# Kernel tuning notes

Hardware: AMD Instinct MI355X
Metric: run time of the kernel (lower is better)

Reference implementation:

```python
import jax, jax.numpy as jnp
import numpy as np

B, S, D = 4, 2048, 1024
H = 16
DH = D // H
MLP_DIM = 4096
EPS = 1e-6


def setup_inputs() -> dict:
    key = jax.random.key(0)
    ks = jax.random.split(key, 16)
    sd = lambda fi, fo: (1.0 / np.sqrt(fi))
    return {
        "x": jax.random.normal(ks[0], (B, S, D), jnp.float32),
        "Wq": jax.random.normal(ks[1], (D, D), jnp.float32) * sd(D, D),
        "bq": jnp.zeros((D,), jnp.float32),
        "Wk": jax.random.normal(ks[2], (D, D), jnp.float32) * sd(D, D),
        "bk": jnp.zeros((D,), jnp.float32),
        "Wv": jax.random.normal(ks[3], (D, D), jnp.float32) * sd(D, D),
        "bv": jnp.zeros((D,), jnp.float32),
        "Wo": jax.random.normal(ks[4], (D, D), jnp.float32) * sd(D, D),
        "bo": jnp.zeros((D,), jnp.float32),
        "ln1_g": jnp.ones((D,), jnp.float32),
        "ln1_b": jnp.zeros((D,), jnp.float32),
        "ln2_g": jnp.ones((D,), jnp.float32),
        "ln2_b": jnp.zeros((D,), jnp.float32),
        "W1": jax.random.normal(ks[5], (D, MLP_DIM), jnp.float32) * sd(D, MLP_DIM),
        "b1": jax.random.normal(ks[6], (MLP_DIM,), jnp.float32) * 1e-6,
        "W2": jax.random.normal(ks[7], (MLP_DIM, D), jnp.float32) * sd(MLP_DIM, D),
        "b2": jax.random.normal(ks[8], (D,), jnp.float32) * 1e-6,
    }


def _layernorm(x, g, b):
    mu = jnp.mean(x, axis=-1, keepdims=True)
    var = jnp.mean(jnp.square(x - mu), axis=-1, keepdims=True)
    return (x - mu) * jax.lax.rsqrt(var + EPS) * g + b


def reference(x, Wq, bq, Wk, bk, Wv, bv, Wo, bo,
              ln1_g, ln1_b, ln2_g, ln2_b, W1, b1, W2, b2):
    h = x
    xn = _layernorm(x, ln1_g, ln1_b)
    # Q/K/V: [B,S,D] -> [B,H,S,DH]
    def split_heads(t):
        return t.reshape(B, S, H, DH).transpose(0, 2, 1, 3)
    Q = split_heads(xn @ Wq + bq)
    K = split_heads(xn @ Wk + bk)
    V = split_heads(xn @ Wv + bv)
    scores = jnp.einsum("bhqd,bhkd->bhqk", Q, K) / np.sqrt(DH).astype(np.float32)
    a = jax.nn.softmax(scores, axis=-1)
    r = jnp.einsum("bhqk,bhkd->bhqd", a, V)          # [B,H,S,DH]
    r = r.transpose(0, 2, 1, 3).reshape(B, S, D)      # merge heads
    r = r @ Wo + bo
    x = r + h
    h = x
    xn = _layernorm(x, ln2_g, ln2_b)
    m = jax.nn.gelu(xn @ W1 + b1, approximate=False)
    m = m @ W2 + b2
    return m + h
```

## Files before the change

kernel.cpp:

```cpp
#include <hip/hip_runtime.h>
#include <math.h>

#define B_ 4
#define S_ 2048
#define D_ 1024
#define H_ 16
#define MLP_ 4096
#define MROWS 8192

typedef __attribute__((ext_vector_type(4))) float f32x4;
typedef __attribute__((ext_vector_type(8))) __bf16 bf16x8;
typedef __attribute__((ext_vector_type(4))) __bf16 bf16x4;
typedef __attribute__((ext_vector_type(8))) unsigned short us8;
typedef unsigned short u16;
typedef unsigned int u32;

__device__ __forceinline__ void gload16(const void* g, void* l) {
    __builtin_amdgcn_global_load_lds((const __attribute__((address_space(1))) u32*)g,
                                     (__attribute__((address_space(3))) u32*)l, 16, 0, 0);
}

__device__ __forceinline__ float gelu_f(float v) {
    return 0.5f * v * (1.0f + erff(v * 0.70710678118654752f));
}

__global__ __launch_bounds__(256) void ln_bf16_k(const float* __restrict__ x,
                                                 const float* __restrict__ g,
                                                 const float* __restrict__ b,
                                                 u16* __restrict__ y) {
    int row = blockIdx.x;
    int tid = threadIdx.x;
    const float* xr = x + (size_t)row * D_;
    f32x4 v = *(const f32x4*)(xr + tid * 4);
    float s = v.x + v.y + v.z + v.w;
    float ss = v.x * v.x + v.y * v.y + v.z * v.z + v.w * v.w;
    for (int off = 32; off > 0; off >>= 1) {
        s += __shfl_down(s, off, 64);
        ss += __shfl_down(ss, off, 64);
    }
    __shared__ float rs[4], rss[4];
    int lane = tid & 63, wid = tid >> 6;
    if (lane == 0) { rs[wid] = s; rss[wid] = ss; }
    __syncthreads();
    s = rs[0] + rs[1] + rs[2] + rs[3];
    ss = rss[0] + rss[1] + rss[2] + rss[3];
    float mu = s * (1.0f / D_);
    float var = ss * (1.0f / D_) - mu * mu;
    float inv = rsqrtf(var + 1e-6f);
    f32x4 gg = *(const f32x4*)(g + tid * 4);
    f32x4 bb = *(const f32x4*)(b + tid * 4);
    bf16x4 o = {(__bf16)((v.x - mu) * inv * gg.x + bb.x),
                (__bf16)((v.y - mu) * inv * gg.y + bb.y),
                (__bf16)((v.z - mu) * inv * gg.z + bb.z),
                (__bf16)((v.w - mu) * inv * gg.w + bb.w)};
    *(bf16x4*)(y + (size_t)row * D_ + tid * 4) = o;
}

__global__ void pack3_k(const float* __restrict__ a, const float* __restrict__ b,
                        const float* __restrict__ c, float* __restrict__ o) {
    const float* s = blockIdx.x == 0 ? a : (blockIdx.x == 1 ? b : c);
    o[blockIdx.x * 1024 + threadIdx.x] = s[threadIdx.x];
}

__global__ __launch_bounds__(256) void wtrans_k(const float* __restrict__ W,
                                                u16* __restrict__ Wt, int K, int N) {
    __shared__ float T[32][33];
    int tid = threadIdx.x;
    int k0 = blockIdx.y * 32, n0 = blockIdx.x * 32;
    int r = tid >> 3, c4 = (tid & 7) * 4;
    f32x4 v = *(const f32x4*)&W[(size_t)(k0 + r) * N + n0 + c4];
    T[r][c4 + 0] = v.x; T[r][c4 + 1] = v.y; T[r][c4 + 2] = v.z; T[r][c4 + 3] = v.w;
    __syncthreads();
    int n = tid >> 3, kk = (tid & 7) * 4;
    bf16x4 o = {(__bf16)T[kk + 0][n], (__bf16)T[kk + 1][n],
                (__bf16)T[kk + 2][n], (__bf16)T[kk + 3][n]};
    *(bf16x4*)&Wt[(size_t)(n0 + n) * K + k0 + kk] = o;
}

__global__ __launch_bounds__(256) void vtrans_k(const u16* __restrict__ QKV,
                                                u16* __restrict__ Vt) {
    __shared__ u16 T[64][80];
    int tid = threadIdx.x;
    int s0 = blockIdx.x * 64;
    int bh = blockIdx.y, b = bh >> 4, h = bh & 15;
    int r = tid >> 2, c0 = (tid & 3) * 16;
    const u16* src = QKV + (size_t)(b * S_ + s0 + r) * 3072 + 2048 + h * 64 + c0;
    us8 v0 = *(const us8*)src;
    us8 v1 = *(const us8*)(src + 8);
    *(us8*)&T[r][c0] = v0;
    *(us8*)&T[r][c0 + 8] = v1;
    __syncthreads();
    int dh = tid >> 2, s8 = (tid & 3) * 16;
    us8 o0, o1;
#pragma unroll
    for (int i = 0; i < 8; ++i) { o0[i] = T[s8 + i][dh]; o1[i] = T[s8 + 8 + i][dh]; }
    u16* dst = Vt + (size_t)(bh * 64 + dh) * S_ + s0 + s8;
    *(us8*)dst = o0;
    *(us8*)(dst + 8) = o1;
}

template <int EPI>
__global__ __launch_bounds__(256) void gemm_bf16(const u16* __restrict__ A,
                                                 const u16* __restrict__ Wt,
                                                 const float* __restrict__ bias,
                                                 const float* __restrict__ res,
                                                 void* __restrict__ Cout,
                                                 int M, int N, int K) {
    __shared__ u16 As[3][128 * 32];
    __shared__ u16 Bs[3][128 * 32];
    const int tid = threadIdx.x;
    const int lane = tid & 63;
    const int w = tid >> 6;
    const int nwg = gridDim.x * gridDim.y;
    int hw = blockIdx.x + gridDim.x * blockIdx.y;
    int lg = (hw & 7) * (nwg >> 3) + (hw >> 3);
    const int row0 = (lg / gridDim.x) * 128;
    const int col0 = (lg % gridDim.x) * 128;
    const int l15 = lane & 15, l16 = lane >> 4;
    const int wr = w >> 1, wc = w & 1;

    f32x4 acc[4][4];
#pragma unroll
    for (int i = 0; i < 4; ++i)
#pragma unroll
        for (int j = 0; j < 4; ++j) acc[i][j] = (f32x4){0.f, 0.f, 0.f, 0.f};

    const int srow = w * 32 + (lane >> 2);
    const size_t sboff = (size_t)(lane & 3) * 16;
    const char* Ag = (const char*)A + ((size_t)(row0 + srow) * K) * 2 + sboff;
    const char* Bg = (const char*)Wt + ((size_t)(col0 + srow) * K) * 2 + sboff;
    const size_t rstep = (size_t)16 * K * 2;
    const int woff = w * 2048;
    const int T = K >> 5;

#define STAGE(t, bi) do {                                      \
        size_t kb = (size_t)(t) << 6;                          \
        char* asw = (char*)As + (bi) * 8192 + woff;            \
        char* bsw = (char*)Bs + (bi) * 8192 + woff;            \
        gload16(Ag + kb, asw);                                 \
        gload16(Ag + kb + rstep, asw + 1024);                  \
        gload16(Bg + kb, bsw);                                 \
        gload16(Bg + kb + rstep, bsw + 1024);                  \
    } while (0)

    STAGE(0, 0);
    STAGE(1, 1);
    asm volatile("s_waitcnt vmcnt(4)" ::: "memory");
    __builtin_amdgcn_s_barrier();
    __builtin_amdgcn_sched_barrier(0);

    int bi = 0;
    for (int t = 0; t < T; ++t) {
        if (t + 2 < T) {
            int nb = bi + 2; if (nb >= 3) nb -= 3;
            STAGE(t + 2, nb);
        }
        const char* Ab = (const char*)As + bi * 8192;
        const char* Bb = (const char*)Bs + bi * 8192;
        bf16x8 af[4], bfr[4];
#pragma unroll
        for (int f = 0; f < 4; ++f) {
            af[f] = *(const bf16x8*)(Ab + (size_t)(wr * 64 + f * 16 + l15) * 64 + (l16 << 4));
            bfr[f] = *(const bf16x8*)(Bb + (size_t)(wc * 64 + f * 16 + l15) * 64 + (l16 << 4));
        }
        __builtin_amdgcn_s_setprio(1);
#pragma unroll
        for (int fi = 0; fi < 4; ++fi)
#pragma unroll
            for (int fj = 0; fj < 4; ++fj)
                acc[fi][fj] = __builtin_amdgcn_mfma_f32_16x16x32_bf16(af[fi], bfr[fj], acc[fi][fj], 0, 0, 0);
        __builtin_amdgcn_s_setprio(0);
        if (t + 2 < T) {
            asm volatile("s_waitcnt vmcnt(4)" ::: "memory");
        } else {
            asm volatile("s_waitcnt vmcnt(0)" ::: "memory");
        }
        __builtin_amdgcn_s_barrier();
        __builtin_amdgcn_sched_barrier(0);
        if (++bi >= 3) bi = 0;
    }
#undef STAGE

    const int rb = row0 + wr * 64 + (l16 << 2);
    const int cb = col0 + wc * 64 + l15;
#pragma unroll
    for (int fi = 0; fi < 4; ++fi)
#pragma unroll
        for (int fj = 0; fj < 4; ++fj) {
            int c = cb + fj * 16;
            float bv = bias[c];
#pragma unroll
            for (int rr = 0; rr < 4; ++rr) {
                int r = rb + fi * 16 + rr;
                float v = acc[fi][fj][rr] + bv;
                if (EPI == 1) v = gelu_f(v);
                if (EPI == 2) {
                    v += res[(size_t)r * N + c];
                    ((float*)Cout)[(size_t)r * N + c] = v;
                } else {
                    ((__bf16*)Cout)[(size_t)r * N + c] = (__bf16)v;
                }
            }
        }
}

__global__ __launch_bounds__(256) void attn_mfma(const u16* __restrict__ QKV,
                                                 const u16* __restrict__ Vt,
                                                 u16* __restrict__ O) {
    __shared__ u16 Ks[2][64 * 64];
    __shared__ u16 Vs[2][64 * 64];
    __shared__ u16 Ps[4][16 * 64];
    const int tid = threadIdx.x, lane = tid & 63, w = tid >> 6;
    int hw = blockIdx.x + gridDim.x * blockIdx.y;
    int lg = (hw & 7) * 256 + (hw >> 3);
    const int bh = lg >> 5, b = bh >> 4, h = bh & 15;
    const int q0 = (lg & 31) * 64;
    const int l15 = lane & 15, l16 = lane >> 4;

    const u16* Qp = QKV + (size_t)(b * S_ + q0 + w * 16 + l15) * 3072 + h * 64 + (l16 << 3);
    bf16x8 qf0 = *(const bf16x8*)Qp;
    bf16x8 qf1 = *(const bf16x8*)(Qp + 32);

    f32x4 oacc[4];
#pragma unroll
    for (int i = 0; i < 4; ++i) oacc[i] = (f32x4){0.f, 0.f, 0.f, 0.f};
    float mold_l = -1e30f, lsum_l = 0.f;

    const int sr = lane >> 3;
    const size_t soff = (size_t)(((lane & 7) ^ sr) << 4);
    const char* Kg = (const char*)QKV + ((size_t)b * S_ * 3072 + 1024 + h * 64) * 2;
    const char* Vg = (const char*)Vt + (size_t)bh * 64 * S_ * 2;
    char* Pw = (char*)Ps[w];
    const float C2 = 0.18033688011112f;
    const float THRRAW = 44.0f;

    const char* kp0 = Kg + (size_t)(w * 16 + sr) * 6144 + soff;
    const char* kp1 = kp0 + 8 * 6144;
    const char* vp0 = Vg + (size_t)(w * 16 + sr) * 4096 + soff;
    const char* vp1 = vp0 + 8 * 4096;
    const size_t KADV = 64 * 6144;
    const size_t VADV = 128;
    char* ksA = (char*)Ks[0] + w * 2048;
    char* ksB = (char*)Ks[1] + w * 2048;
    char* vsA = (char*)Vs[0] + w * 2048;
    char* vsB = (char*)Vs[1] + w * 2048;

    gload16(kp0, ksA); gload16(kp1, ksA + 1024);
    gload16(vp0, vsA); gload16(vp1, vsA + 1024);
    kp0 += KADV; kp1 += KADV; vp0 += VADV; vp1 += VADV;
    __syncthreads();

    for (int kt = 0; kt < S_ / 64; ++kt) {
        const int cur = kt & 1;
        if (kt < S_ / 64 - 1) {
            char* kd = cur ? ksA : ksB;
            char* vd = cur ? vsA : vsB;
            gload16(kp0, kd); gload16(kp1, kd + 1024);
            gload16(vp0, vd); gload16(vp1, vd + 1024);
            kp0 += KADV; kp1 += KADV; vp0 += VADV; vp1 += VADV;
        }

        f32x4 sfr[4];
        const char* Kb_ = (const char*)Ks[cur];
        __builtin_amdgcn_s_setprio(1);
#pragma unroll
        for (int cf = 0; cf < 4; ++cf) {
            int r = cf * 16 + l15;
            int x0 = (l16 << 4) ^ ((r & 7) << 4);
            bf16x8 k0v = *(const bf16x8*)(Kb_ + r * 128 + x0);
            bf16x8 k1v = *(const bf16x8*)(Kb_ + r * 128 + (x0 ^ 64));
            f32x4 t = (f32x4){0.f, 0.f, 0.f, 0.f};
            t = __builtin_amdgcn_mfma_f32_16x16x32_bf16(k0v, qf0, t, 0, 0, 0);
            t = __builtin_amdgcn_mfma_f32_16x16x32_bf16(k1v, qf1, t, 0, 0, 0);
            sfr[cf] = t;
        }
        __builtin_amdgcn_s_setprio(0);

        float mx = fmaxf(fmaxf(sfr[0][0], sfr[0][1]), sfr[0][2]);
        mx = fmaxf(fmaxf(mx, sfr[0][3]), sfr[1][0]);
        mx = fmaxf(fmaxf(mx, sfr[1][1]), sfr[1][2]);
        mx = fmaxf(fmaxf(mx, sfr[1][3]), sfr[2][0]);
        mx = fmaxf(fmaxf(mx, sfr[2][1]), sfr[2][2]);
        mx = fmaxf(fmaxf(mx, sfr[2][3]), sfr[3][0]);
        mx = fmaxf(fmaxf(mx, sfr[3][1]), sfr[3][2]);
        mx = fmaxf(mx, sfr[3][3]);
        mx = fmaxf(mx, __shfl_xor(mx, 16, 64));
        mx = fmaxf(mx, __shfl_xor(mx, 32, 64));

        bool need = mx > mold_l + THRRAW;
        if (__any(need)) {
            float mnew = fmaxf(mold_l, mx);
            float al = exp2f((mold_l - mnew) * C2);
            lsum_l *= al;
            mold_l = mnew;
#pragma unroll
            for (int rr = 0; rr < 4; ++rr) {
                float alq = __shfl(al, (l16 << 2) + rr, 64);
#pragma unroll
                for (int fj = 0; fj < 4; ++fj) oacc[fj][rr] *= alq;
            }
        }

        float nm = -mold_l * C2;
        float pv[4][4];
        float psum = 0.f;
#pragma unroll
        for (int cf = 0; cf < 4; ++cf)
#pragma unroll
            for (int rr = 0; rr < 4; ++rr) {
                float p = exp2f(fmaf(sfr[cf][rr], C2, nm));
                pv[cf][rr] = p;
                psum += p;
            }
        psum += __shfl_xor(psum, 16, 64);
        psum += __shfl_xor(psum, 32, 64);
        lsum_l += psum;

        {
            char* Pr = Pw + l15 * 128;
            const int sw = (l15 & 7) << 4;
#pragma unroll
            for (int cf = 0; cf < 4; ++cf) {
                bf16x4 pk = {(__bf16)pv[cf][0], (__bf16)pv[cf][1],
                             (__bf16)pv[cf][2], (__bf16)pv[cf][3]};
                *(bf16x4*)(Pr + ((cf * 32 + l16 * 8) ^ sw)) = pk;
            }
        }

        {
            const char* Vb_ = (const char*)Vs[cur];
            int x0 = (l16 << 4) ^ ((l15 & 7) << 4);
            bf16x8 pf0 = *(const bf16x8*)(Pw + l15 * 128 + x0);
            bf16x8 pf1 = *(const bf16x8*)(Pw + l15 * 128 + (x0 ^ 64));
            __builtin_amdgcn_s_setprio(1);
#pragma unroll
            for (int fj = 0; fj < 4; ++fj) {
                int vr = fj * 16 + l15;
                int y0 = (l16 << 4) ^ ((vr & 7) << 4);
                bf16x8 v0 = *(const bf16x8*)(Vb_ + vr * 128 + y0);
                bf16x8 v1 = *(const bf16x8*)(Vb_ + vr * 128 + (y0 ^ 64));
                oacc[fj] = __builtin_amdgcn_mfma_f32_16x16x32_bf16(pf0, v0, oacc[fj], 0, 0, 0);
                oacc[fj] = __builtin_amdgcn_mfma_f32_16x16x32_bf16(pf1, v1, oacc[fj], 0, 0, 0);
            }
            __builtin_amdgcn_s_setprio(0);
        }
        __syncthreads();
    }

    float inv_l = 1.0f / lsum_l;
    float invq[4];
#pragma unroll
    for (int rr = 0; rr < 4; ++rr) invq[rr] = __shfl(inv_l, (l16 << 2) + rr, 64);
#pragma unroll
    for (int fj = 0; fj < 4; ++fj)
#pragma unroll
        for (int rr = 0; rr < 4; ++rr) {
            int r = b * S_ + q0 + w * 16 + (l16 << 2) + rr;
            ((__bf16*)O)[(size_t)r * D_ + h * 64 + fj * 16 + l15] = (__bf16)(oacc[fj][rr] * invq[rr]);
        }
}

extern "C" void kernel_launch(void* const* d_in, const int* in_sizes, int n_in,
                              void* d_out, int out_size, void* d_ws, size_t ws_size,
                              hipStream_t stream) {
    const float* x     = (const float*)d_in[0];
    const float* Wq    = (const float*)d_in[1];
    const float* bq    = (const float*)d_in[2];
    const float* Wk    = (const float*)d_in[3];
    const float* bk    = (const float*)d_in[4];
    const float* Wv    = (const float*)d_in[5];
    const float* bv    = (const float*)d_in[6];
    const float* Wo    = (const float*)d_in[7];
    const float* bo    = (const float*)d_in[8];
    const float* ln1_g = (const float*)d_in[9];
    const float* ln1_b = (const float*)d_in[10];
    const float* ln2_g = (const float*)d_in[11];
    const float* ln2_b = (const float*)d_in[12];
    const float* W1    = (const float*)d_in[13];
    const float* b1    = (const float*)d_in[14];
    const float* W2    = (const float*)d_in[15];
    const float* b2    = (const float*)d_in[16];
    float* out = (float*)d_out;

    const size_t MB = 1ull << 20;
    char* ws = (char*)d_ws;
    u16* QKVb = (u16*)(ws + 0 * MB);
    u16* aout = (u16*)(ws + 48 * MB);
    u16* mid  = (u16*)(ws + 0 * MB);
    float* x2 = (float*)(ws + 64 * MB);
    float* bqkv = (float*)(ws + 64 * MB);
    u16* xn   = (u16*)(ws + 96 * MB);
    u16* Vt   = (u16*)(ws + 96 * MB);
    u16* xn2  = (u16*)(ws + 96 * MB);
    u16* Wqkvt = (u16*)(ws + 112 * MB);
    u16* Wot  = Wqkvt + (size_t)3072 * D_;
    u16* W1t  = (u16*)(ws + 112 * MB);
    u16* W2t  = (u16*)(ws + 120 * MB);

    wtrans_k<<<dim3(32, 32), 256, 0, stream>>>(Wq, Wqkvt, D_, D_);
    wtrans_k<<<dim3(32, 32), 256, 0, stream>>>(Wk, Wqkvt + (size_t)D_ * D_, D_, D_);
    wtrans_k<<<dim3(32, 32), 256, 0, stream>>>(Wv, Wqkvt + (size_t)2 * D_ * D_, D_, D_);
    wtrans_k<<<dim3(32, 32), 256, 0, stream>>>(Wo, Wot, D_, D_);
    wtrans_k<<<dim3(32, 128), 256, 0, stream>>>(W2, W2t, MLP_, D_);
    pack3_k<<<3, 1024, 0, stream>>>(bq, bk, bv, bqkv);

    ln_bf16_k<<<MROWS, 256, 0, stream>>>(x, ln1_g, ln1_b, xn);
    gemm_bf16<0><<<dim3(24, 64), 256, 0, stream>>>(xn, Wqkvt, bqkv, nullptr, QKVb, MROWS, 3072, D_);
    vtrans_k<<<dim3(32, 64), 256, 0, stream>>>(QKVb, Vt);
    attn_mfma<<<dim3(32, 64), 256, 0, stream>>>(QKVb, Vt, aout);
    gemm_bf16<2><<<dim3(8, 64), 256, 0, stream>>>(aout, Wot, bo, x, x2, MROWS, D_, D_);
    wtrans_k<<<dim3(128, 32), 256, 0, stream>>>(W1, W1t, D_, MLP_);
    ln_bf16_k<<<MROWS, 256, 0, stream>>>(x2, ln2_g, ln2_b, xn2);
    gemm_bf16<1><<<dim3(32, 64), 256, 0, stream>>>(xn2, W1t, b1, nullptr, mid, MROWS, MLP_, D_);
    gemm_bf16<2><<<dim3(8, 64), 256, 0, stream>>>(mid, W2t, b2, x2, (void*)out, MROWS, D_, MLP_);
}
```

Measured before the change: 504.0 us.

## Switch attention to 32x32x16 MFMA with 128-row query tiles per block

Rewrites the attention kernel to use 32x32x16 bf16 MFMA instead of 16x16x32. Each wave now owns 32 query rows, so a block covers 128 queries and the grid is halved. This reuses each K/V tile loaded into LDS across twice as many queries, removes the per-row shuffles of the softmax scale, and writes output rows contiguously as bf16x4. In exchange it needs more accumulator registers per wave and twice the P scratch in LDS, which may reduce occupancy.

Result: no change. 504.0 us (-0.0%).

```diff
diff --git a/kernel.cpp b/kernel.cpp
--- a/kernel.cpp
+++ b/kernel.cpp
@@ -9,6 +9,7 @@
 #define MROWS 8192
 
 typedef __attribute__((ext_vector_type(4))) float f32x4;
+typedef __attribute__((ext_vector_type(16))) float f32x16;
 typedef __attribute__((ext_vector_type(8))) __bf16 bf16x8;
 typedef __attribute__((ext_vector_type(4))) __bf16 bf16x4;
 typedef __attribute__((ext_vector_type(8))) unsigned short us8;
@@ -209,28 +210,32 @@
                                                  u16* __restrict__ O) {
     __shared__ u16 Ks[2][64 * 64];
     __shared__ u16 Vs[2][64 * 64];
-    __shared__ u16 Ps[4][16 * 64];
+    __shared__ u16 Ps[4][32 * 64];
     const int tid = threadIdx.x, lane = tid & 63, w = tid >> 6;
     int hw = blockIdx.x + gridDim.x * blockIdx.y;
-    int lg = (hw & 7) * 256 + (hw >> 3);
-    const int bh = lg >> 5, b = bh >> 4, h = bh & 15;
-    const int q0 = (lg & 31) * 64;
-    const int l15 = lane & 15, l16 = lane >> 4;
-
-    const u16* Qp = QKV + (size_t)(b * S_ + q0 + w * 16 + l15) * 3072 + h * 64 + (l16 << 3);
-    bf16x8 qf0 = *(const bf16x8*)Qp;
-    bf16x8 qf1 = *(const bf16x8*)(Qp + 32);
-
-    f32x4 oacc[4];
-#pragma unroll
-    for (int i = 0; i < 4; ++i) oacc[i] = (f32x4){0.f, 0.f, 0.f, 0.f};
-    float mold_l = -1e30f, lsum_l = 0.f;
+    int lg = (hw & 7) * 128 + (hw >> 3);
+    const int bh = lg >> 4, b = bh >> 4, h = bh & 15;
+    const int q0 = (lg & 15) * 128;
+    const int l31 = lane & 31, lh = lane >> 5;
+
+    const u16* Qp = QKV + (size_t)(b * S_ + q0 + w * 32 + l31) * 3072 + h * 64 + lh * 8;
+    bf16x8 qf[4];
+    qf[0] = *(const bf16x8*)(Qp);
+    qf[1] = *(const bf16x8*)(Qp + 16);
+    qf[2] = *(const bf16x8*)(Qp + 32);
+    qf[3] = *(const bf16x8*)(Qp + 48);
+
+    f32x16 oacc[2];
+#pragma unroll
+    for (int i = 0; i < 16; ++i) { oacc[0][i] = 0.f; oacc[1][i] = 0.f; }
+    float mold = -1e30f, lsum = 0.f;
 
     const int sr = lane >> 3;
     const size_t soff = (size_t)(((lane & 7) ^ sr) << 4);
     const char* Kg = (const char*)QKV + ((size_t)b * S_ * 3072 + 1024 + h * 64) * 2;
     const char* Vg = (const char*)Vt + (size_t)bh * 64 * S_ * 2;
     char* Pw = (char*)Ps[w];
+    const int sw = (l31 & 7) << 4;
     const float C2 = 0.18033688011112f;
     const float THRRAW = 44.0f;
 
@@ -260,103 +265,103 @@
             kp0 += KADV; kp1 += KADV; vp0 += VADV; vp1 += VADV;
         }
 
-        f32x4 sfr[4];
         const char* Kb_ = (const char*)Ks[cur];
+        f32x16 sfr[2];
         __builtin_amdgcn_s_setprio(1);
 #pragma unroll
-        for (int cf = 0; cf < 4; ++cf) {
-            int r = cf * 16 + l15;
-            int x0 = (l16 << 4) ^ ((r & 7) << 4);
-            bf16x8 k0v = *(const bf16x8*)(Kb_ + r * 128 + x0);
-            bf16x8 k1v = *(const bf16x8*)(Kb_ + r * 128 + (x0 ^ 64));
-            f32x4 t = (f32x4){0.f, 0.f, 0.f, 0.f};
-            t = __builtin_amdgcn_mfma_f32_16x16x32_bf16(k0v, qf0, t, 0, 0, 0);
-            t = __builtin_amdgcn_mfma_f32_16x16x32_bf16(k1v, qf1, t, 0, 0, 0);
-            sfr[cf] = t;
+        for (int kh = 0; kh < 2; ++kh) {
+            int r = kh * 32 + l31;
+            int rsw = (r & 7) << 4;
+            const char* Kr = Kb_ + r * 128;
+            f32x16 t;
+#pragma unroll
+            for (int i = 0; i < 16; ++i) t[i] = 0.f;
+#pragma unroll
+            for (int ds = 0; ds < 4; ++ds) {
+                bf16x8 kf = *(const bf16x8*)(Kr + ((((ds * 2 + lh) << 4)) ^ rsw));
+                t = __builtin_amdgcn_mfma_f32_32x32x16_bf16(kf, qf[ds], t, 0, 0, 0);
+            }
+            sfr[kh] = t;
         }
         __builtin_amdgcn_s_setprio(0);
 
-        float mx = fmaxf(fmaxf(sfr[0][0], sfr[0][1]), sfr[0][2]);
-        mx = fmaxf(fmaxf(mx, sfr[0][3]), sfr[1][0]);
-        mx = fmaxf(fmaxf(mx, sfr[1][1]), sfr[1][2]);
-        mx = fmaxf(fmaxf(mx, sfr[1][3]), sfr[2][0]);
-        mx = fmaxf(fmaxf(mx, sfr[2][1]), sfr[2][2]);
-        mx = fmaxf(fmaxf(mx, sfr[2][3]), sfr[3][0]);
-        mx = fmaxf(fmaxf(mx, sfr[3][1]), sfr[3][2]);
-        mx = fmaxf(mx, sfr[3][3]);
-        mx = fmaxf(mx, __shfl_xor(mx, 16, 64));
+        float mx = fmaxf(sfr[0][0], sfr[1][0]);
+#pragma unroll
+        for (int i = 1; i < 16; ++i) mx = fmaxf(mx, fmaxf(sfr[0][i], sfr[1][i]));
         mx = fmaxf(mx, __shfl_xor(mx, 32, 64));
 
-        bool need = mx > mold_l + THRRAW;
+        bool need = mx > mold + THRRAW;
         if (__any(need)) {
-            float mnew = fmaxf(mold_l, mx);
-            float al = exp2f((mold_l - mnew) * C2);
-            lsum_l *= al;
-            mold_l = mnew;
-#pragma unroll
-            for (int rr = 0; rr < 4; ++rr) {
-                float alq = __shfl(al, (l16 << 2) + rr, 64);
-#pragma unroll
-                for (int fj = 0; fj < 4; ++fj) oacc[fj][rr] *= alq;
-            }
-        }
-
-        float nm = -mold_l * C2;
-        float pv[4][4];
+            float mnew = fmaxf(mold, mx);
+            float al = exp2f((mold - mnew) * C2);
+            lsum *= al;
+            mold = mnew;
+#pragma unroll
+            for (int i = 0; i < 16; ++i) { oacc[0][i] *= al; oacc[1][i] *= al; }
+        }
+
+        float nm = -mold * C2;
+        float pv0[16], pv1[16];
         float psum = 0.f;
 #pragma unroll
-        for (int cf = 0; cf < 4; ++cf)
-#pragma unroll
-            for (int rr = 0; rr < 4; ++rr) {
-                float p = exp2f(fmaf(sfr[cf][rr], C2, nm));
-                pv[cf][rr] = p;
-                psum += p;
-            }
-        psum += __shfl_xor(psum, 16, 64);
+        for (int i = 0; i < 16; ++i) {
+            pv0[i] = exp2f(fmaf(sfr[0][i], C2, nm));
+            pv1[i] = exp2f(fmaf(sfr[1][i], C2, nm));
+            psum += pv0[i] + pv1[i];
+        }
         psum += __shfl_xor(psum, 32, 64);
-        lsum_l += psum;
+        lsum += psum;
 
         {
-            char* Pr = Pw + l15 * 128;
-            const int sw = (l15 & 7) << 4;
-#pragma unroll
-            for (int cf = 0; cf < 4; ++cf) {
-                bf16x4 pk = {(__bf16)pv[cf][0], (__bf16)pv[cf][1],
-                             (__bf16)pv[cf][2], (__bf16)pv[cf][3]};
-                *(bf16x4*)(Pr + ((cf * 32 + l16 * 8) ^ sw)) = pk;
+            char* Pr = Pw + l31 * 128;
+#pragma unroll
+            for (int t4 = 0; t4 < 4; ++t4) {
+                int kb0 = (t4 * 8 + lh * 4) * 2;
+                bf16x4 pa = {(__bf16)pv0[t4 * 4], (__bf16)pv0[t4 * 4 + 1],
+                             (__bf16)pv0[t4 * 4 + 2], (__bf16)pv0[t4 * 4 + 3]};
+                bf16x4 pb = {(__bf16)pv1[t4 * 4], (__bf16)pv1[t4 * 4 + 1],
+                             (__bf16)pv1[t4 * 4 + 2], (__bf16)pv1[t4 * 4 + 3]};
+                *(bf16x4*)(Pr + (kb0 ^ sw)) = pa;
+                *(bf16x4*)(Pr + ((kb0 + 64) ^ sw)) = pb;
             }
         }
 
         {
             const char* Vb_ = (const char*)Vs[cur];
-            int x0 = (l16 << 4) ^ ((l15 & 7) << 4);
-            bf16x8 pf0 = *(const bf16x8*)(Pw + l15 * 128 + x0);
-            bf16x8 pf1 = *(const bf16x8*)(Pw + l15 * 128 + (x0 ^ 64));
+            const char* Pr = Pw + l31 * 128;
+            bf16x8 pf[4];
+#pragma unroll
+            for (int ks = 0; ks < 4; ++ks)
+                pf[ks] = *(const bf16x8*)(Pr + ((((ks * 2 + lh) << 4)) ^ sw));
             __builtin_amdgcn_s_setprio(1);
 #pragma unroll
-            for (int fj = 0; fj < 4; ++fj) {
-                int vr = fj * 16 + l15;
-                int y0 = (l16 << 4) ^ ((vr & 7) << 4);
-                bf16x8 v0 = *(const bf16x8*)(Vb_ + vr * 128 + y0);
-                bf16x8 v1 = *(const bf16x8*)(Vb_ + vr * 128 + (y0 ^ 64));
-                oacc[fj] = __builtin_amdgcn_mfma_f32_16x16x32_bf16(pf0, v0, oacc[fj], 0, 0, 0);
-                oacc[fj] = __builtin_amdgcn_mfma_f32_16x16x32_bf16(pf1, v1, oacc[fj], 0, 0, 0);
+            for (int dh = 0; dh < 2; ++dh) {
+                int r = dh * 32 + l31;
+                int rsw = (r & 7) << 4;
+                const char* Vr = Vb_ + r * 128;
+#pragma unroll
+                for (int ks = 0; ks < 4; ++ks) {
+                    bf16x8 vf = *(const bf16x8*)(Vr + ((((ks * 2 + lh) << 4)) ^ rsw));
+                    oacc[dh] = __builtin_amdgcn_mfma_f32_32x32x16_bf16(vf, pf[ks], oacc[dh], 0, 0, 0);
+                }
             }
             __builtin_amdgcn_s_setprio(0);
         }
         __syncthreads();
     }
 
-    float inv_l = 1.0f / lsum_l;
-    float invq[4];
-#pragma unroll
-    for (int rr = 0; rr < 4; ++rr) invq[rr] = __shfl(inv_l, (l16 << 2) + rr, 64);
-#pragma unroll
-    for (int fj = 0; fj < 4; ++fj)
-#pragma unroll
-        for (int rr = 0; rr < 4; ++rr) {
-            int r = b * S_ + q0 + w * 16 + (l16 << 2) + rr;
-            ((__bf16*)O)[(size_t)r * D_ + h * 64 + fj * 16 + l15] = (__bf16)(oacc[fj][rr] * invq[rr]);
+    float invl = 1.0f / lsum;
+    char* Og = (char*)O + ((size_t)(b * S_ + q0 + w * 32 + l31) * 1024 + h * 64) * 2;
+#pragma unroll
+    for (int dh = 0; dh < 2; ++dh)
+#pragma unroll
+        for (int t4 = 0; t4 < 4; ++t4) {
+            int db = dh * 32 + t4 * 8 + lh * 4;
+            bf16x4 ov = {(__bf16)(oacc[dh][t4 * 4] * invl),
+                         (__bf16)(oacc[dh][t4 * 4 + 1] * invl),
+                         (__bf16)(oacc[dh][t4 * 4 + 2] * invl),
+                         (__bf16)(oacc[dh][t4 * 4 + 3] * invl)};
+            *(bf16x4*)(Og + db * 2) = ov;
         }
 }
 
@@ -407,7 +412,7 @@
     ln_bf16_k<<<MROWS, 256, 0, stream>>>(x, ln1_g, ln1_b, xn);
     gemm_bf16<0><<<dim3(24, 64), 256, 0, stream>>>(xn, Wqkvt, bqkv, nullptr, QKVb, MROWS, 3072, D_);
     vtrans_k<<<dim3(32, 64), 256, 0, stream>>>(QKVb, Vt);
-    attn_mfma<<<dim3(32, 64), 256, 0, stream>>>(QKVb, Vt, aout);
+    attn_mfma<<<dim3(16, 64), 256, 0, stream>>>(QKVb, Vt, aout);
     gemm_bf16<2><<<dim3(8, 64), 256, 0, stream>>>(aout, Wot, bo, x, x2, MROWS, D_, D_);
     wtrans_k<<<dim3(128, 32), 256, 0, stream>>>(W1, W1t, D_, MLP_);
     ln_bf16_k<<<MROWS, 256, 0, stream>>>(x2, ln2_g, ln2_b, xn2);
```
